# Performance work log

Hardware: AMD Instinct MI355X
Metric: run time of the kernel (lower is better)

## Reference

```python
import jax, jax.numpy as jnp
import numpy as np

N = 20000            # nodes
E = 320000           # edges (before self loops)
NUM_PLAYERS = 5000
FEAT = 64            # feature_dim
H = 128              # hidden_dim
OUT = 10             # out_features
NEG_SLOPE = 0.2


def _p(key, shape, fan_in):
    return jax.random.normal(key, shape, dtype=jnp.float32) / np.sqrt(fan_in)


def setup_inputs() -> dict:
    key = jax.random.key(0)
    ks = jax.random.split(key, 20)
    # x_player: col 0 = player id (stored as float), cols 1: = features
    ids = jax.random.randint(ks[0], (N, 1), 0, NUM_PLAYERS + 1).astype(jnp.float32)
    feats = jax.random.normal(ks[1], (N, FEAT), dtype=jnp.float32)
    x_player = jnp.concatenate([ids, feats], axis=1)
    edge_index = jax.random.randint(ks[2], (2, E), 0, N, dtype=jnp.int32)
    return {
        "x_player": x_player,
        "edge_index": edge_index,
        "emb": jax.random.normal(ks[3], (NUM_PLAYERS + 1, H), dtype=jnp.float32),
        "proj_W": _p(ks[4], (H + FEAT, H), H + FEAT),
        "proj_b": jnp.zeros((H,), jnp.float32),
        "W1l": _p(ks[5], (H, 4 * H), H),
        "W1r": _p(ks[6], (H, 4 * H), H),
        "att1": _p(ks[7], (4, H), H),
        "b1": jnp.zeros((4 * H,), jnp.float32),
        "W2l": _p(ks[8], (4 * H, H), 4 * H),
        "W2r": _p(ks[9], (4 * H, H), 4 * H),
        "att2": _p(ks[10], (1, H), H),
        "b2": jnp.zeros((H,), jnp.float32),
        "out_W": _p(ks[11], (H, OUT), H),
        "out_b": jnp.zeros((OUT,), jnp.float32),
    }


def gatv2(x, src, dst, Wl, Wr, att, bias, heads, ch, concat):
    # GATv2Conv (PyG defaults: share_weights=False, negative_slope=0.2,
    # add_self_loops handled by caller, dropout off at eval)
    xl = (x @ Wl).reshape(N, heads, ch)   # source transform (x_j)
    xr = (x @ Wr).reshape(N, heads, ch)   # target transform (x_i)
    h = xl[src] + xr[dst]                                      # [E,H,C]
    e = jnp.sum(jax.nn.leaky_relu(h, NEG_SLOPE) * att, -1)     # [E,H]
    # segment softmax over incoming edges of each dst node
    m = jax.ops.segment_max(e, dst, num_segments=N)            # [N,H]
    ex = jnp.exp(e - m[dst])
    s = jax.ops.segment_sum(ex, dst, num_segments=N)
    alpha = ex / (s[dst] + 1e-16)                              # [E,H]
    out = jax.ops.segment_sum(alpha[..., None] * xl[src], dst, num_segments=N)
    out = out.reshape(N, heads * ch) if concat else out.mean(axis=1)
    return out + bias


def reference(x_player, edge_index, emb, proj_W, proj_b,
              W1l, W1r, att1, b1, W2l, W2r, att2, b2, out_W, out_b):
    ids = x_player[:, 0].astype(jnp.int32)
    combined = jnp.concatenate([emb[ids], x_player[:, 1:]], axis=1)
    x = jax.nn.relu(combined @ proj_W + proj_b)                # [N,H]
    # add self loops (GATv2Conv default)
    loop = jnp.arange(N, dtype=edge_index.dtype)
    src = jnp.concatenate([edge_index[0], loop])
    dst = jnp.concatenate([edge_index[1], loop])
    x = jax.nn.relu(gatv2(x, src, dst, W1l, W1r, att1, b1, 4, H, True))
    x = gatv2(x, src, dst, W2l, W2r, att2, b2, 1, H, True)
    return x @ out_W + out_b                                   # [N,OUT]
```

## Files before the change

### kernel.cpp

```cpp
#include <hip/hip_runtime.h>
#include <math.h>

#define NNODES 20000
#define XP_COLS 65

typedef unsigned int uint32;
typedef __attribute__((ext_vector_type(8))) short short8;
typedef __attribute__((ext_vector_type(4))) float float4v;

__device__ __forceinline__ float bflo(uint32 u){ return __uint_as_float(u << 16); }
__device__ __forceinline__ float bfhi(uint32 u){ return __uint_as_float(u & 0xffff0000u); }
__device__ __forceinline__ unsigned short f2bf(float f){
  uint32 u = __float_as_uint(f);
  uint32 r = (u + 0x7fffu + ((u >> 16) & 1u)) >> 16;
  return (unsigned short)r;
}
__device__ __forceinline__ void unpack8(uint4 u, float* x){
  x[0]=bflo(u.x); x[1]=bfhi(u.x); x[2]=bflo(u.y); x[3]=bfhi(u.y);
  x[4]=bflo(u.z); x[5]=bfhi(u.z); x[6]=bflo(u.w); x[7]=bfhi(u.w);
}
__device__ __forceinline__ float rowsum16(float x){
  x += __int_as_float(__builtin_amdgcn_update_dpp(0, __float_as_int(x), 0x121, 0xf, 0xf, true));
  x += __int_as_float(__builtin_amdgcn_update_dpp(0, __float_as_int(x), 0x122, 0xf, 0xf, true));
  x += __int_as_float(__builtin_amdgcn_update_dpp(0, __float_as_int(x), 0x124, 0xf, 0xf, true));
  x += __int_as_float(__builtin_amdgcn_update_dpp(0, __float_as_int(x), 0x128, 0xf, 0xf, true));
  return x;
}

__global__ void k_cvt_count(const int* __restrict__ dst, int E, int* __restrict__ deg,
                            const float* __restrict__ W1l, const float* __restrict__ W1r,
                            const float* __restrict__ W2l, const float* __restrict__ W2r,
                            const float* __restrict__ projW,
                            unsigned short* __restrict__ T1l, unsigned short* __restrict__ T1r,
                            unsigned short* __restrict__ T2l, unsigned short* __restrict__ T2r,
                            unsigned short* __restrict__ Tp){
  int gid = blockIdx.x * 256 + threadIdx.x;
  if (gid < E){
    atomicAdd(&deg[dst[gid]], 1);
    return;
  }
  int idx = gid - E;
  if (idx < 65536){
    int o = idx;
    int n = o >> 7, k = o & 127;
    T1l[o] = f2bf(W1l[k * 512 + n]);
  } else if (idx < 131072){
    int o = idx - 65536;
    int n = o >> 7, k = o & 127;
    T1r[o] = f2bf(W1r[k * 512 + n]);
  } else if (idx < 196608){
    int o = idx - 131072;
    int n = o >> 9, k = o & 511;
    T2l[o] = f2bf(W2l[k * 128 + n]);
  } else if (idx < 262144){
    int o = idx - 196608;
    int n = o >> 9, k = o & 511;
    T2r[o] = f2bf(W2r[k * 128 + n]);
  } else if (idx < 286720){
    int o = idx - 262144;
    int n = o / 192, k = o - n * 192;
    Tp[o] = f2bf(projW[k * 128 + n]);
  }
}

__global__ __launch_bounds__(256) void k_scan(const int* __restrict__ deg,
                                              int* __restrict__ off,
                                              int* __restrict__ cursor){
  const int CH = 80;
  int tid = threadIdx.x;
  int lane = tid & 63, w = tid >> 6;
  int beg = tid * CH;
  bool act = beg < NNODES;
  int sum = 0;
  if (act){
    const int4* p = (const int4*)(deg + beg);
    #pragma unroll
    for (int i = 0; i < 20; i++){
      int4 v = p[i];
      sum += v.x + v.y + v.z + v.w + 4;
    }
  }
  int inc = sum;
  #pragma unroll
  for (int d = 1; d < 64; d <<= 1){
    int t = __shfl_up(inc, d, 64);
    if (lane >= d) inc += t;
  }
  __shared__ int wtot[4];
  if (lane == 63) wtot[w] = inc;
  __syncthreads();
  int wbase = 0;
  for (int i = 0; i < w; i++) wbase += wtot[i];
  int run = wbase + inc - sum;
  if (act){
    const int4* p = (const int4*)(deg + beg);
    int4* po = (int4*)(off + beg);
    int4* pc = (int4*)(cursor + beg);
    #pragma unroll
    for (int i = 0; i < 20; i++){
      int4 v = p[i];
      int4 o;
      o.x = run; run += v.x + 1;
      o.y = run; run += v.y + 1;
      o.z = run; run += v.z + 1;
      o.w = run; run += v.w + 1;
      po[i] = o; pc[i] = o;
    }
  }
  if (tid == 249) off[NNODES] = run;
}

__global__ void k_fill(const int* __restrict__ src, const int* __restrict__ dst, int E,
                       int* __restrict__ cursor, int* __restrict__ csr){
  int t = blockIdx.x * 256 + threadIdx.x;
  if (t < NNODES){
    int p = atomicAdd(&cursor[t], 1);
    csr[p] = t;
  } else if (t < NNODES + E){
    int e = t - NNODES;
    int p = atomicAdd(&cursor[dst[e]], 1);
    csr[p] = src[e];
  }
}

__global__ __launch_bounds__(256) void k_proj_mfma(const float* __restrict__ xp,
                                                   const float* __restrict__ emb,
                                                   const unsigned short* __restrict__ Bt,
                                                   const float* __restrict__ bias,
                                                   unsigned short* __restrict__ Xb){
  __shared__ unsigned short As[64][40];
  __shared__ unsigned short Bs[128][40];
  __shared__ int ids[64];
  int tid = threadIdx.x;
  int bm = blockIdx.x * 64;
  int w = tid >> 6, lane = tid & 63;
  int wm = (w >> 1) * 32, wn = (w & 1) * 64;
  int quad = lane >> 4, l16 = lane & 15;
  if (tid < 64){
    int g = bm + tid;
    ids[tid] = (g < NNODES) ? (int)xp[(size_t)g * XP_COLS] : 0;
  }
  float4v acc[2][4];
  #pragma unroll
  for (int i = 0; i < 2; i++)
    #pragma unroll
    for (int j = 0; j < 4; j++) acc[i][j] = (float4v){0.f,0.f,0.f,0.f};
  int am = tid >> 2, ak = (tid & 3) * 8;
  int gm = bm + am;
  bool mv = gm < NNODES;
  int brow = tid >> 1, bk = (tid & 1) * 16;
  __syncthreads();

  for (int k0 = 0; k0 < 192; k0 += 32){
    float v[8];
    if (k0 < 128){
      const float* ep = emb + (size_t)ids[am] * 128 + k0 + ak;
      float4 e0 = *(const float4*)ep;
      float4 e1 = *(const float4*)(ep + 4);
      v[0]=e0.x; v[1]=e0.y; v[2]=e0.z; v[3]=e0.w;
      v[4]=e1.x; v[5]=e1.y; v[6]=e1.z; v[7]=e1.w;
    } else {
      const float* fp = xp + (size_t)gm * XP_COLS + 1 + (k0 - 128) + ak;
      #pragma unroll
      for (int i = 0; i < 8; i++) v[i] = mv ? fp[i] : 0.f;
    }
    ushort4 o0, o1;
    o0.x=f2bf(v[0]); o0.y=f2bf(v[1]); o0.z=f2bf(v[2]); o0.w=f2bf(v[3]);
    o1.x=f2bf(v[4]); o1.y=f2bf(v[5]); o1.z=f2bf(v[6]); o1.w=f2bf(v[7]);
    *(ushort4*)&As[am][ak]     = o0;
    *(ushort4*)&As[am][ak + 4] = o1;
    const unsigned short* bp = Bt + (size_t)brow * 192 + k0 + bk;
    *(uint4*)&Bs[brow][bk]     = *(const uint4*)bp;
    *(uint4*)&Bs[brow][bk + 8] = *(const uint4*)(bp + 8);
    __syncthreads();
    short8 af[2], bf[4];
    #pragma unroll
    for (int t = 0; t < 2; t++) af[t] = *(const short8*)&As[wm + t * 16 + l16][quad * 8];
    #pragma unroll
    for (int t = 0; t < 4; t++) bf[t] = *(const short8*)&Bs[wn + t * 16 + l16][quad * 8];
    #pragma unroll
    for (int tm = 0; tm < 2; tm++)
      #pragma unroll
      for (int tn = 0; tn < 4; tn++)
        acc[tm][tn] = __builtin_amdgcn_mfma_f32_16x16x32_bf16(af[tm], bf[tn], acc[tm][tn], 0, 0, 0);
    __syncthreads();
  }
  #pragma unroll
  for (int tm = 0; tm < 2; tm++){
    #pragma unroll
    for (int r = 0; r < 4; r++){
      int row = bm + wm + tm * 16 + quad * 4 + r;
      if (row >= NNODES) continue;
      #pragma unroll
      for (int tn = 0; tn < 4; tn++){
        int col = wn + tn * 16 + l16;
        float val = fmaxf(acc[tm][tn][r] + bias[col], 0.f);
        Xb[(size_t)row * 128 + col] = f2bf(val);
      }
    }
  }
}

template<int K, int N, int MODE, int NH>
__global__ __launch_bounds__(256) void k_mfma(const unsigned short* __restrict__ A,
                                              const unsigned short* __restrict__ B0t,
                                              const unsigned short* __restrict__ B1t,
                                              void* __restrict__ C0, void* __restrict__ C1,
                                              const float* __restrict__ att,
                                              float* __restrict__ dl, float* __restrict__ dr,
                                              int* __restrict__ gmax){
  const unsigned short* Bt = blockIdx.z ? B1t : B0t;
  __shared__ unsigned short As[64][40];
  __shared__ unsigned short Bs[128][40];
  __shared__ float red[4][32];
  __shared__ float redu[4][32];
  int tid = threadIdx.x;
  int bm = blockIdx.y * 64;
  int bn = blockIdx.x * 128;
  int head = (NH == 1) ? 0 : blockIdx.x;
  int w = tid >> 6, lane = tid & 63;
  int wm = (w >> 1) * 32, wn = (w & 1) * 64;
  int quad = lane >> 4, l16 = lane & 15;
  float av[4], aav[4];
  #pragma unroll
  for (int tn = 0; tn < 4; tn++){
    av[tn] = att[head * 128 + wn + tn * 16 + l16];
    aav[tn] = fabsf(av[tn]);
  }
  float4v acc[2][4];
  #pragma unroll
  for (int i = 0; i < 2; i++)
    #pragma unroll
    for (int j = 0; j < 4; j++) acc[i][j] = (float4v){0.f,0.f,0.f,0.f};
  int am = tid >> 2, ak = (tid & 3) * 8;
  int gm = bm + am;
  bool mv = gm < NNODES;
  int brow = tid >> 1, bk = (tid & 1) * 16;

  for (int k0 = 0; k0 < K; k0 += 32){
    uint4 va = {0u,0u,0u,0u};
    if (mv) va = *(const uint4*)(A + (size_t)gm * K + k0 + ak);
    *(uint4*)&As[am][ak] = va;
    const unsigned short* bp = Bt + (size_t)(bn + brow) * K + k0 + bk;
    *(uint4*)&Bs[brow][bk]     = *(const uint4*)bp;
    *(uint4*)&Bs[brow][bk + 8] = *(const uint4*)(bp + 8);
    __syncthreads();
    short8 af[2], bf[4];
    #pragma unroll
    for (int t = 0; t < 2; t++) af[t] = *(const short8*)&As[wm + t * 16 + l16][quad * 8];
    #pragma unroll
    for (int t = 0; t < 4; t++) bf[t] = *(const short8*)&Bs[wn + t * 16 + l16][quad * 8];
    #pragma unroll
    for (int tm = 0; tm < 2; tm++)
      #pragma unroll
      for (int tn = 0; tn < 4; tn++)
        acc[tm][tn] = __builtin_amdgcn_mfma_f32_16x16x32_bf16(af[tm], bf[tn], acc[tm][tn], 0, 0, 0);
    __syncthreads();
  }
  #pragma unroll
  for (int tm = 0; tm < 2; tm++){
    #pragma unroll
    for (int r = 0; r < 4; r++){
      int row = bm + wm + tm * 16 + quad * 4 + r;
      if (row < NNODES){
        #pragma unroll
        for (int tn = 0; tn < 4; tn++){
          int col = bn + wn + tn * 16 + l16;
          float val = acc[tm][tn][r];
          if (MODE == 0 || blockIdx.z == 0){
            unsigned short* C = (unsigned short*)(blockIdx.z ? C1 : C0);
            C[(size_t)row * N + col] = f2bf(val);
          } else {
            ((float*)C1)[(size_t)row * N + col] = val;
          }
        }
      }
      float pd = acc[tm][0][r] * av[0];
      pd = fmaf(acc[tm][1][r], av[1], pd);
      pd = fmaf(acc[tm][2][r], av[2], pd);
      pd = fmaf(acc[tm][3][r], av[3], pd);
      float pu = fabsf(acc[tm][0][r]) * aav[0];
      pu = fmaf(fabsf(acc[tm][1][r]), aav[1], pu);
      pu = fmaf(fabsf(acc[tm][2][r]), aav[2], pu);
      pu = fmaf(fabsf(acc[tm][3][r]), aav[3], pu);
      pd = rowsum16(pd);
      pu = rowsum16(pu);
      if (l16 == 0){
        red[w][tm * 16 + quad * 4 + r]  = pd;
        redu[w][tm * 16 + quad * 4 + r] = pu;
      }
    }
  }
  __syncthreads();
  if (tid < 64){
    float vd, vu;
    if (tid < 32){ vd = red[0][tid] + red[1][tid];   vu = redu[0][tid] + redu[1][tid]; }
    else { vd = red[2][tid & 31] + red[3][tid & 31]; vu = redu[2][tid & 31] + redu[3][tid & 31]; }
    int row = bm + tid;
    bool ok = row < NNODES;
    if (ok){
      float* D = blockIdx.z ? dr : dl;
      D[row * NH + head] = vd;
    }
    if (blockIdx.z == 0){
      float v = ok ? fmaf(0.4f, vu, 0.6f * vd) : -4.0e6f;
      #pragma unroll
      for (int dd = 1; dd < 64; dd <<= 1) v = fmaxf(v, __shfl_xor(v, dd));
      if (tid == 0) atomicMax(&gmax[head], (int)ceilf(v * 256.0f) + (1 << 30));
    }
  }
}

__device__ __forceinline__ void attn1_batch(const uint4* u, const float* d,
                                            const float* r, const float* a, float base,
                                            float& s, float* acc){
  float x0[8], x1[8], x2[8], x3[8];
  unpack8(u[0], x0); unpack8(u[1], x1); unpack8(u[2], x2); unpack8(u[3], x3);
  float p0 = 0.f, p1 = 0.f, p2 = 0.f, p3 = 0.f;
  #pragma unroll
  for (int i = 0; i < 8; i++){
    p0 = fmaf(a[i], fabsf(x0[i] + r[i]), p0);
    p1 = fmaf(a[i], fabsf(x1[i] + r[i]), p1);
    p2 = fmaf(a[i], fabsf(x2[i] + r[i]), p2);
    p3 = fmaf(a[i], fabsf(x3[i] + r[i]), p3);
  }
  p0 = rowsum16(p0); p1 = rowsum16(p1); p2 = rowsum16(p2); p3 = rowsum16(p3);
  float ex0 = __expf(fmaf(0.4f, p0, fmaf(0.6f, d[0], base)));
  float ex1 = __expf(fmaf(0.4f, p1, fmaf(0.6f, d[1], base)));
  float ex2 = __expf(fmaf(0.4f, p2, fmaf(0.6f, d[2], base)));
  float ex3 = __expf(fmaf(0.4f, p3, fmaf(0.6f, d[3], base)));
  s += (ex0 + ex1) + (ex2 + ex3);
  #pragma unroll
  for (int i = 0; i < 8; i++){
    float t = fmaf(ex0, x0[i], ex1 * x1[i]);
    t = fmaf(ex2, x2[i], t);
    acc[i] = fmaf(ex3, x3[i], acc[i] + t);
  }
}

__global__ __launch_bounds__(1024) void k_attn1(const unsigned short* __restrict__ xl,
                                                const unsigned short* __restrict__ xr,
                                                const float* __restrict__ dl, const float* __restrict__ dr,
                                                const float* __restrict__ att, const float* __restrict__ bias,
                                                const int* __restrict__ gmax,
                                                const int* __restrict__ off, const int* __restrict__ csr,
                                                unsigned short* __restrict__ out){
  int lane = threadIdx.x & 63;
  int n = blockIdx.x * 16 + (threadIdx.x >> 6);
  int h = lane >> 4;
  uint4 ur = *(const uint4*)(xr + (size_t)n * 512 + lane * 8);
  float r[8]; unpack8(ur, r);
  const float* ap = att + lane * 8;
  float4 A0 = *(const float4*)ap, A1 = *(const float4*)(ap + 4);
  float a[8] = {A0.x,A0.y,A0.z,A0.w,A1.x,A1.y,A1.z,A1.w};
  float V = 0.f;
  #pragma unroll
  for (int i = 0; i < 8; i++) V = fmaf(fabsf(a[i]), fabsf(r[i]), V);
  V = rowsum16(V);
  float Mg = (float)(gmax[h] - (1 << 30)) * (1.0f / 256.0f);
  float base = fmaf(0.6f, dr[n * 4 + h], -Mg - 0.4f * V);
  int beg = off[n], end = off[n + 1];
  int cnt = end - beg;
  int nfull = cnt >> 2;

  float s = 0.f;
  float acc[8] = {0,0,0,0,0,0,0,0};
  uint4 uA[4], uB[4];
  float dA[4], dB[4];
  int j = beg;
  if (nfull > 0){
    int s0 = csr[j], s1 = csr[j+1], s2 = csr[j+2], s3 = csr[j+3];
    uA[0] = *(const uint4*)(xl + (size_t)s0 * 512 + lane * 8);
    uA[1] = *(const uint4*)(xl + (size_t)s1 * 512 + lane * 8);
    uA[2] = *(const uint4*)(xl + (size_t)s2 * 512 + lane * 8);
    uA[3] = *(const uint4*)(xl + (size_t)s3 * 512 + lane * 8);
    dA[0] = dl[s0*4+h]; dA[1] = dl[s1*4+h]; dA[2] = dl[s2*4+h]; dA[3] = dl[s3*4+h];
  }
  for (int b = 0; b < nfull; b++){
    int jn = j + 4;
    if (b + 1 < nfull){
      int s0 = csr[jn], s1 = csr[jn+1], s2 = csr[jn+2], s3 = csr[jn+3];
      uB[0] = *(const uint4*)(xl + (size_t)s0 * 512 + lane * 8);
      uB[1] = *(const uint4*)(xl + (size_t)s1 * 512 + lane * 8);
      uB[2] = *(const uint4*)(xl + (size_t)s2 * 512 + lane * 8);
      uB[3] = *(const uint4*)(xl + (size_t)s3 * 512 + lane * 8);
      dB[0] = dl[s0*4+h]; dB[1] = dl[s1*4+h]; dB[2] = dl[s2*4+h]; dB[3] = dl[s3*4+h];
    }
    attn1_batch(uA, dA, r, a, base, s, acc);
    j = jn;
    #pragma unroll
    for (int i = 0; i < 4; i++){ uA[i] = uB[i]; dA[i] = dB[i]; }
  }
  for (; j < end; j++){
    int sn = csr[j];
    float dls = dl[sn * 4 + h];
    uint4 ux = *(const uint4*)(xl + (size_t)sn * 512 + lane * 8);
    float x[8]; unpack8(ux, x);
    float pa = 0.f, pb = 0.f;
    #pragma unroll
    for (int i = 0; i < 4; i++){
      pa = fmaf(a[i],     fabsf(x[i]     + r[i]),     pa);
      pb = fmaf(a[i + 4], fabsf(x[i + 4] + r[i + 4]), pb);
    }
    float p = rowsum16(pa + pb);
    float ex = __expf(fmaf(0.4f, p, fmaf(0.6f, dls, base)));
    s += ex;
    #pragma unroll
    for (int i = 0; i < 8; i++) acc[i] = fmaf(ex, x[i], acc[i]);
  }
  float inv = 1.f / (s + 1e-16f);
  const float* bp = bias + lane * 8;
  float4 B0 = *(const float4*)bp, B1 = *(const float4*)(bp + 4);
  float bb[8] = {B0.x,B0.y,B0.z,B0.w,B1.x,B1.y,B1.z,B1.w};
  unsigned short o[8];
  #pragma unroll
  for (int i = 0; i < 8; i++)
    o[i] = f2bf(fmaxf(fmaf(acc[i], inv, bb[i]), 0.f));
  uint4 ov;
  ov.x = (uint32)o[0] | ((uint32)o[1] << 16);
  ov.y = (uint32)o[2] | ((uint32)o[3] << 16);
  ov.z = (uint32)o[4] | ((uint32)o[5] << 16);
  ov.w = (uint32)o[6] | ((uint32)o[7] << 16);
  *(uint4*)(out + (size_t)n * 512 + lane * 8) = ov;
}

__device__ __forceinline__ float red64(float p){
  p = rowsum16(p);
  p += __shfl_xor(p, 16);
  p += __shfl_xor(p, 32);
  return p;
}
__device__ __forceinline__ void attn2_batch(const uint32* u, const float* d,
                                            float2 rv, float2 av, float base,
                                            float& s, float& a0, float& a1){
  float x00 = bflo(u[0]), x01 = bfhi(u[0]);
  float x10 = bflo(u[1]), x11 = bfhi(u[1]);
  float x20 = bflo(u[2]), x21 = bfhi(u[2]);
  float x30 = bflo(u[3]), x31 = bfhi(u[3]);
  float p0 = fmaf(av.x, fabsf(x00 + rv.x), av.y * fabsf(x01 + rv.y));
  float p1 = fmaf(av.x, fabsf(x10 + rv.x), av.y * fabsf(x11 + rv.y));
  float p2 = fmaf(av.x, fabsf(x20 + rv.x), av.y * fabsf(x21 + rv.y));
  float p3 = fmaf(av.x, fabsf(x30 + rv.x), av.y * fabsf(x31 + rv.y));
  p0 = red64(p0); p1 = red64(p1); p2 = red64(p2); p3 = red64(p3);
  float ex0 = __expf(fmaf(0.4f, p0, fmaf(0.6f, d[0], base)));
  float ex1 = __expf(fmaf(0.4f, p1, fmaf(0.6f, d[1], base)));
  float ex2 = __expf(fmaf(0.4f, p2, fmaf(0.6f, d[2], base)));
  float ex3 = __expf(fmaf(0.4f, p3, fmaf(0.6f, d[3], base)));
  s += (ex0 + ex1) + (ex2 + ex3);
  float t0 = fmaf(ex0, x00, ex1 * x10); t0 = fmaf(ex2, x20, t0);
  float t1 = fmaf(ex0, x01, ex1 * x11); t1 = fmaf(ex2, x21, t1);
  a0 = fmaf(ex3, x30, a0 + t0);
  a1 = fmaf(ex3, x31, a1 + t1);
}

__global__ __launch_bounds__(1024) void k_attn2(const unsigned short* __restrict__ xl,
                                                const float* __restrict__ xr,
                                                const float* __restrict__ dl, const float* __restrict__ dr,
                                                const float* __restrict__ att, const float* __restrict__ bias,
                                                const float* __restrict__ outW, const float* __restrict__ outb,
                                                const int* __restrict__ gmax,
                                                const int* __restrict__ off, const int* __restrict__ csr,
                                                float* __restrict__ out){
  __shared__ float Wsh[1280];
  int tid = threadIdx.x;
  for (int i = tid; i < 1280; i += 1024) Wsh[i] = outW[i];
  __syncthreads();
  int lane = tid & 63;
  int n = blockIdx.x * 16 + (tid >> 6);
  float2 rv = *(const float2*)(xr + (size_t)n * 128 + lane * 2);
  float2 av = *(const float2*)(att + lane * 2);
  float V = red64(fmaf(fabsf(av.x), fabsf(rv.x), fabsf(av.y) * fabsf(rv.y)));
  float Mg = (float)(gmax[0] - (1 << 30)) * (1.0f / 256.0f);
  float base = fmaf(0.6f, dr[n], -Mg - 0.4f * V);
  int beg = off[n], end = off[n + 1];
  int cnt = end - beg;
  int nfull = cnt >> 2;
  float s = 0.f;
  float a0 = 0.f, a1 = 0.f;
  uint32 uA[4], uB[4];
  float dA[4], dB[4];
  int j = beg;
  if (nfull > 0){
    int s0 = csr[j], s1 = csr[j+1], s2 = csr[j+2], s3 = csr[j+3];
    uA[0] = *(const uint32*)(xl + (size_t)s0 * 128 + lane * 2);
    uA[1] = *(const uint32*)(xl + (size_t)s1 * 128 + lane * 2);
    uA[2] = *(const uint32*)(xl + (size_t)s2 * 128 + lane * 2);
    uA[3] = *(const uint32*)(xl + (size_t)s3 * 128 + lane * 2);
    dA[0] = dl[s0]; dA[1] = dl[s1]; dA[2] = dl[s2]; dA[3] = dl[s3];
  }
  for (int b = 0; b < nfull; b++){
    int jn = j + 4;
    if (b + 1 < nfull){
      int s0 = csr[jn], s1 = csr[jn+1], s2 = csr[jn+2], s3 = csr[jn+3];
      uB[0] = *(const uint32*)(xl + (size_t)s0 * 128 + lane * 2);
      uB[1] = *(const uint32*)(xl + (size_t)s1 * 128 + lane * 2);
      uB[2] = *(const uint32*)(xl + (size_t)s2 * 128 + lane * 2);
      uB[3] = *(const uint32*)(xl + (size_t)s3 * 128 + lane * 2);
      dB[0] = dl[s0]; dB[1] = dl[s1]; dB[2] = dl[s2]; dB[3] = dl[s3];
    }
    attn2_batch(uA, dA, rv, av, base, s, a0, a1);
    j = jn;
    #pragma unroll
    for (int i = 0; i < 4; i++){ uA[i] = uB[i]; dA[i] = dB[i]; }
  }
  for (; j < end; j++){
    int sn = csr[j];
    float dls = dl[sn];
    uint32 u = *(const uint32*)(xl + (size_t)sn * 128 + lane * 2);
    float x0 = bflo(u), x1 = bfhi(u);
    float p = red64(fmaf(av.x, fabsf(x0 + rv.x), av.y * fabsf(x1 + rv.y)));
    float ex = __expf(fmaf(0.4f, p, fmaf(0.6f, dls, base)));
    s += ex;
    a0 = fmaf(ex, x0, a0);
    a1 = fmaf(ex, x1, a1);
  }
  float inv = 1.f / (s + 1e-16f);
  int c = lane * 2;
  float x2_0 = fmaf(a0, inv, bias[c]);
  float x2_1 = fmaf(a1, inv, bias[c + 1]);
  #pragma unroll
  for (int o = 0; o < 10; o++){
    float p = fmaf(x2_0, Wsh[c * 10 + o], x2_1 * Wsh[(c + 1) * 10 + o]);
    p = red64(p);
    if (lane == 0) out[(size_t)n * 10 + o] = p + outb[o];
  }
}

extern "C" void kernel_launch(void* const* d_in, const int* in_sizes, int n_in,
                              void* d_out, int out_size, void* d_ws, size_t ws_size,
                              hipStream_t stream){
  const float* xp    = (const float*)d_in[0];
  const int*   ei    = (const int*)  d_in[1];
  const float* emb   = (const float*)d_in[2];
  const float* projW = (const float*)d_in[3];
  const float* projb = (const float*)d_in[4];
  const float* W1l   = (const float*)d_in[5];
  const float* W1r   = (const float*)d_in[6];
  const float* att1  = (const float*)d_in[7];
  const float* b1    = (const float*)d_in[8];
  const float* W2l   = (const float*)d_in[9];
  const float* W2r   = (const float*)d_in[10];
  const float* att2  = (const float*)d_in[11];
  const float* b2    = (const float*)d_in[12];
  const float* outW  = (const float*)d_in[13];
  const float* outb  = (const float*)d_in[14];
  float* out = (float*)d_out;

  int E = in_sizes[1] / 2;
  const int* esrc = ei;
  const int* edst = ei + E;

  char* w = (char*)d_ws;
  int* gmaxi = (int*)w; w += 32;
  int* deg  = (int*)w; w += (size_t)NNODES * 4;
  int* off  = (int*)w; w += (size_t)(NNODES + 4) * 4;
  int* cur  = (int*)w; w += (size_t)NNODES * 4;
  int* csr  = (int*)w; w += (size_t)(NNODES + E) * 4;
  unsigned short* Xb   = (unsigned short*)w; w += (size_t)NNODES * 128 * 2;
  unsigned short* Wt1l = (unsigned short*)w; w += (size_t)512 * 128 * 2;
  unsigned short* Wt1r = (unsigned short*)w; w += (size_t)512 * 128 * 2;
  unsigned short* Wt2l = (unsigned short*)w; w += (size_t)128 * 512 * 2;
  unsigned short* Wt2r = (unsigned short*)w; w += (size_t)128 * 512 * 2;
  unsigned short* Wtp  = (unsigned short*)w; w += (size_t)128 * 192 * 2;
  unsigned short* xl1b = (unsigned short*)w; w += (size_t)NNODES * 512 * 2;
  unsigned short* xr1b = (unsigned short*)w; w += (size_t)NNODES * 512 * 2;
  unsigned short* X1b  = (unsigned short*)w; w += (size_t)NNODES * 512 * 2;
  unsigned short* xl2b = (unsigned short*)w; w += (size_t)NNODES * 128 * 2;
  float* xr2 = (float*)w; w += (size_t)NNODES * 128 * 4;
  float* dl1 = (float*)w; w += (size_t)NNODES * 4 * 4;
  float* dr1 = (float*)w; w += (size_t)NNODES * 4 * 4;
  float* dl2 = (float*)w; w += (size_t)NNODES * 4;
  float* dr2 = (float*)w; w += (size_t)NNODES * 4;

  hipMemsetAsync(gmaxi, 0, 32 + (size_t)NNODES * 4, stream);
  int cvt_total = E + 286720;
  k_cvt_count<<<(cvt_total + 255) / 256, 256, 0, stream>>>(
      edst, E, deg, W1l, W1r, W2l, W2r, projW, Wt1l, Wt1r, Wt2l, Wt2r, Wtp);
  k_scan<<<1, 256, 0, stream>>>(deg, off, cur);
  k_fill<<<(NNODES + E + 255) / 256, 256, 0, stream>>>(esrc, edst, E, cur, csr);

  k_proj_mfma<<<dim3((NNODES + 63) / 64), 256, 0, stream>>>(xp, emb, Wtp, projb, Xb);
  k_mfma<128, 512, 0, 4><<<dim3(4, (NNODES + 63) / 64, 2), 256, 0, stream>>>(
      Xb, Wt1l, Wt1r, xl1b, xr1b, att1, dl1, dr1, gmaxi);
  k_attn1<<<NNODES / 16, 1024, 0, stream>>>(xl1b, xr1b, dl1, dr1, att1, b1, gmaxi, off, csr, X1b);
  k_mfma<512, 128, 1, 1><<<dim3(1, (NNODES + 63) / 64, 2), 256, 0, stream>>>(
      X1b, Wt2l, Wt2r, xl2b, xr2, att2, dl2, dr2, gmaxi + 4);
  k_attn2<<<NNODES / 16, 1024, 0, stream>>>(xl2b, xr2, dl2, dr2, att2, b2, outW, outb, gmaxi + 4, off, csr, out);
}
```

Before: 287.5 us.

## Record edge ranks at count time, tile weight transposes, shrink attn1 blocks

The degree-count atomic now returns each edge's rank within its destination, so CSR fill becomes a plain scatter to off[d]+rank with no second round of atomics and no cursor array. Weight transpose/bf16 conversion uses 32x32 shared-memory tiles so both reads and writes are coalesced instead of strided. k_attn1 goes from 1024-thread blocks of 16 nodes to 256-thread blocks of 4 nodes for finer scheduling. It costs an extra E-sized rank buffer, and the CSR order within each segment is still nondeterministic.

```diff
diff --git a/kernel.cpp b/kernel.cpp
--- a/kernel.cpp
+++ b/kernel.cpp
@@ -26,46 +26,53 @@
   x += __int_as_float(__builtin_amdgcn_update_dpp(0, __float_as_int(x), 0x128, 0xf, 0xf, true));
   return x;
 }
-
-__global__ void k_cvt_count(const int* __restrict__ dst, int E, int* __restrict__ deg,
+__device__ __forceinline__ float red64(float p){
+  p = rowsum16(p);
+  p += __shfl_xor(p, 16);
+  p += __shfl_xor(p, 32);
+  return p;
+}
+
+__global__ __launch_bounds__(256) void k_cvt_count(const int* __restrict__ dst, int E, int CB,
+                            int* __restrict__ deg, int* __restrict__ rank,
                             const float* __restrict__ W1l, const float* __restrict__ W1r,
                             const float* __restrict__ W2l, const float* __restrict__ W2r,
                             const float* __restrict__ projW,
                             unsigned short* __restrict__ T1l, unsigned short* __restrict__ T1r,
                             unsigned short* __restrict__ T2l, unsigned short* __restrict__ T2r,
                             unsigned short* __restrict__ Tp){
-  int gid = blockIdx.x * 256 + threadIdx.x;
-  if (gid < E){
-    atomicAdd(&deg[dst[gid]], 1);
+  __shared__ float tile[32][33];
+  int bid = blockIdx.x;
+  if (bid < CB){
+    int e = bid * 256 + threadIdx.x;
+    if (e < E) rank[e] = atomicAdd(&deg[dst[e]], 1);
     return;
   }
-  int idx = gid - E;
-  if (idx < 65536){
-    int o = idx;
-    int n = o >> 7, k = o & 127;
-    T1l[o] = f2bf(W1l[k * 512 + n]);
-  } else if (idx < 131072){
-    int o = idx - 65536;
-    int n = o >> 7, k = o & 127;
-    T1r[o] = f2bf(W1r[k * 512 + n]);
-  } else if (idx < 196608){
-    int o = idx - 131072;
-    int n = o >> 9, k = o & 511;
-    T2l[o] = f2bf(W2l[k * 128 + n]);
-  } else if (idx < 262144){
-    int o = idx - 196608;
-    int n = o >> 9, k = o & 511;
-    T2r[o] = f2bf(W2r[k * 128 + n]);
-  } else if (idx < 286720){
-    int o = idx - 262144;
-    int n = o / 192, k = o - n * 192;
-    Tp[o] = f2bf(projW[k * 128 + n]);
+  int t = bid - CB;
+  const float* S; unsigned short* D;
+  int SK, SN, kt, nt;
+  if (t < 64){        S = W1l; D = T1l; SK = 128; SN = 512; int q = t;        kt = q & 3;  nt = q >> 2; }
+  else if (t < 128){  S = W1r; D = T1r; SK = 128; SN = 512; int q = t - 64;   kt = q & 3;  nt = q >> 2; }
+  else if (t < 192){  S = W2l; D = T2l; SK = 512; SN = 128; int q = t - 128;  kt = q & 15; nt = q >> 4; }
+  else if (t < 256){  S = W2r; D = T2r; SK = 512; SN = 128; int q = t - 192;  kt = q & 15; nt = q >> 4; }
+  else {              S = projW; D = Tp; SK = 192; SN = 128; int q = t - 256; kt = q % 6;  nt = q / 6; }
+  int tid = threadIdx.x;
+  int c = tid & 31, r0 = tid >> 5;
+  #pragma unroll
+  for (int i = 0; i < 4; i++){
+    int r = r0 + i * 8;
+    tile[r][c] = S[(size_t)(kt * 32 + r) * SN + nt * 32 + c];
+  }
+  __syncthreads();
+  #pragma unroll
+  for (int i = 0; i < 4; i++){
+    int r = r0 + i * 8;
+    D[(size_t)(nt * 32 + r) * SK + kt * 32 + c] = f2bf(tile[c][r]);
   }
 }
 
 __global__ __launch_bounds__(256) void k_scan(const int* __restrict__ deg,
-                                              int* __restrict__ off,
-                                              int* __restrict__ cursor){
+                                              int* __restrict__ off){
   const int CH = 80;
   int tid = threadIdx.x;
   int lane = tid & 63, w = tid >> 6;
@@ -95,7 +102,6 @@
   if (act){
     const int4* p = (const int4*)(deg + beg);
     int4* po = (int4*)(off + beg);
-    int4* pc = (int4*)(cursor + beg);
     #pragma unroll
     for (int i = 0; i < 20; i++){
       int4 v = p[i];
@@ -104,22 +110,22 @@
       o.y = run; run += v.y + 1;
       o.z = run; run += v.z + 1;
       o.w = run; run += v.w + 1;
-      po[i] = o; pc[i] = o;
+      po[i] = o;
     }
   }
   if (tid == 249) off[NNODES] = run;
 }
 
 __global__ void k_fill(const int* __restrict__ src, const int* __restrict__ dst, int E,
-                       int* __restrict__ cursor, int* __restrict__ csr){
+                       const int* __restrict__ off, const int* __restrict__ deg,
+                       const int* __restrict__ rank, int* __restrict__ csr){
   int t = blockIdx.x * 256 + threadIdx.x;
-  if (t < NNODES){
-    int p = atomicAdd(&cursor[t], 1);
-    csr[p] = t;
-  } else if (t < NNODES + E){
-    int e = t - NNODES;
-    int p = atomicAdd(&cursor[dst[e]], 1);
-    csr[p] = src[e];
+  if (t < E){
+    int d = dst[t];
+    csr[off[d] + rank[t]] = src[t];
+  } else if (t < E + NNODES){
+    int n = t - E;
+    csr[off[n] + deg[n]] = n;
   }
 }
 
@@ -338,15 +344,15 @@
   }
 }
 
-__global__ __launch_bounds__(1024) void k_attn1(const unsigned short* __restrict__ xl,
-                                                const unsigned short* __restrict__ xr,
-                                                const float* __restrict__ dl, const float* __restrict__ dr,
-                                                const float* __restrict__ att, const float* __restrict__ bias,
-                                                const int* __restrict__ gmax,
-                                                const int* __restrict__ off, const int* __restrict__ csr,
-                                                unsigned short* __restrict__ out){
+__global__ __launch_bounds__(256) void k_attn1(const unsigned short* __restrict__ xl,
+                                               const unsigned short* __restrict__ xr,
+                                               const float* __restrict__ dl, const float* __restrict__ dr,
+                                               const float* __restrict__ att, const float* __restrict__ bias,
+                                               const int* __restrict__ gmax,
+                                               const int* __restrict__ off, const int* __restrict__ csr,
+                                               unsigned short* __restrict__ out){
   int lane = threadIdx.x & 63;
-  int n = blockIdx.x * 16 + (threadIdx.x >> 6);
+  int n = blockIdx.x * 4 + (threadIdx.x >> 6);
   int h = lane >> 4;
   uint4 ur = *(const uint4*)(xr + (size_t)n * 512 + lane * 8);
   float r[8]; unpack8(ur, r);
@@ -424,12 +430,6 @@
   *(uint4*)(out + (size_t)n * 512 + lane * 8) = ov;
 }
 
-__device__ __forceinline__ float red64(float p){
-  p = rowsum16(p);
-  p += __shfl_xor(p, 16);
-  p += __shfl_xor(p, 32);
-  return p;
-}
 __device__ __forceinline__ void attn2_batch(const uint32* u, const float* d,
                                             float2 rv, float2 av, float base,
                                             float& s, float& a0, float& a1){
@@ -554,7 +554,7 @@
   int* gmaxi = (int*)w; w += 32;
   int* deg  = (int*)w; w += (size_t)NNODES * 4;
   int* off  = (int*)w; w += (size_t)(NNODES + 4) * 4;
-  int* cur  = (int*)w; w += (size_t)NNODES * 4;
+  int* rank = (int*)w; w += (size_t)E * 4;
   int* csr  = (int*)w; w += (size_t)(NNODES + E) * 4;
   unsigned short* Xb   = (unsigned short*)w; w += (size_t)NNODES * 128 * 2;
   unsigned short* Wt1l = (unsigned short*)w; w += (size_t)512 * 128 * 2;
@@ -573,16 +573,16 @@
   float* dr2 = (float*)w; w += (size_t)NNODES * 4;
 
   hipMemsetAsync(gmaxi, 0, 32 + (size_t)NNODES * 4, stream);
-  int cvt_total = E + 286720;
-  k_cvt_count<<<(cvt_total + 255) / 256, 256, 0, stream>>>(
-      edst, E, deg, W1l, W1r, W2l, W2r, projW, Wt1l, Wt1r, Wt2l, Wt2r, Wtp);
-  k_scan<<<1, 256, 0, stream>>>(deg, off, cur);
-  k_fill<<<(NNODES + E + 255) / 256, 256, 0, stream>>>(esrc, edst, E, cur, csr);
+  int CB = (E + 255) / 256;
+  k_cvt_count<<<CB + 280, 256, 0, stream>>>(
+      edst, E, CB, deg, rank, W1l, W1r, W2l, W2r, projW, Wt1l, Wt1r, Wt2l, Wt2r, Wtp);
+  k_scan<<<1, 256, 0, stream>>>(deg, off);
+  k_fill<<<(E + NNODES + 255) / 256, 256, 0, stream>>>(esrc, edst, E, off, deg, rank, csr);
 
   k_proj_mfma<<<dim3((NNODES + 63) / 64), 256, 0, stream>>>(xp, emb, Wtp, projb, Xb);
   k_mfma<128, 512, 0, 4><<<dim3(4, (NNODES + 63) / 64, 2), 256, 0, stream>>>(
       Xb, Wt1l, Wt1r, xl1b, xr1b, att1, dl1, dr1, gmaxi);
-  k_attn1<<<NNODES / 16, 1024, 0, stream>>>(xl1b, xr1b, dl1, dr1, att1, b1, gmaxi, off, csr, X1b);
+  k_attn1<<<NNODES / 4, 256, 0, stream>>>(xl1b, xr1b, dl1, dr1, att1, b1, gmaxi, off, csr, X1b);
   k_mfma<512, 128, 1, 1><<<dim3(1, (NNODES + 63) / 64, 2), 256, 0, stream>>>(
       X1b, Wt2l, Wt2r, xl2b, xr2, att2, dl2, dr2, gmaxi + 4);
   k_attn2<<<NNODES / 16, 1024, 0, stream>>>(xl2b, xr2, dl2, dr2, att2, b2, outW, outb, gmaxi + 4, off, csr, out);
```

Measured after the change: 269.3 us. 6.4% less time.
